# Performance work log

Hardware: AMD Instinct MI355X
Metric: run time of the kernel (lower is better)

## Reference

```python
import jax, jax.numpy as jnp
import numpy as np
import math

T_MIN = 0.1
T_MAX = 1.0


def setup_inputs() -> dict:
    key = jax.random.key(0)
    k1, k2, k3, k4, k5, k6 = jax.random.split(key, 6)
    B, H, SQ, SK, DK = 1, 16, 4096, 4096, 64
    query = jax.random.normal(k1, (B, H, SQ, DK), dtype=jnp.float32)
    key_t = jax.random.normal(k2, (B, H, SK, DK), dtype=jnp.float32)
    # MLP params (3 -> 16 -> 1). Original zero-inits the last layer; we use
    # small random values so gradients flow to query/key in the bwd test.
    W1 = jax.random.normal(k3, (16, 3), dtype=jnp.float32) * 0.5
    b1 = jax.random.normal(k4, (16,), dtype=jnp.float32) * 0.1
    W2 = jax.random.normal(k5, (1, 16), dtype=jnp.float32) * 0.5
    b2 = jax.random.normal(k6, (1,), dtype=jnp.float32) * 0.1
    return {"query": query, "key": key_t, "W1": W1, "b1": b1, "W2": W2, "b2": b2}


def reference(query, key, W1, b1, W2, b2):
    d_k = query.shape[-1]
    sk = key.shape[-2]
    q = query.astype(jnp.float32)
    k = key.astype(jnp.float32)
    # [B,H,Sq,Sk] score matrix
    scores = jnp.einsum('bhqd,bhkd->bhqk', q, k) / math.sqrt(d_k)
    scores = jnp.clip(scores, -50.0, 50.0)
    mean_sim = scores.mean(axis=(-2, -1))                 # [B,H]
    max_sim = scores.max(axis=-1).mean(axis=-1)           # [B,H]
    probs = jax.nn.softmax(scores / 2.0, axis=-1)         # [B,H,Sq,Sk]
    # torch .var(dim=-1) is unbiased (divisor Sk-1)
    pm = probs.mean(axis=-1, keepdims=True)
    var = ((probs - pm) ** 2).sum(axis=-1) / (sk - 1)     # [B,H,Sq]
    entropy_proxy = var.mean(axis=-1)                     # [B,H]
    mean_sim = jnp.clip(mean_sim, -10.0, 10.0)
    max_sim = jnp.clip(max_sim, -10.0, 10.0)
    entropy_proxy = jnp.clip(entropy_proxy, 0.0, 1.0)
    features = jnp.stack([mean_sim, max_sim, entropy_proxy], axis=-1)  # [B,H,3]
    h = jnp.tanh(features @ W1.T + b1)
    raw_t = h @ W2.T + b2                                 # [B,H,1]
    t = T_MIN + jax.nn.sigmoid(raw_t) * (T_MAX - T_MIN)
    t = jnp.clip(t, T_MIN, T_MAX)
    return t[..., None].astype(query.dtype)               # [B,H,1,1]
```

## Files before the change

### kernel.cpp

```cpp
#include <hip/hip_runtime.h>
#include <math.h>

#define NH   16
#define SQL  4096
#define SKL  4096
#define DK   64
#define QB   128
#define KB   64
#define KSPLIT 2
#define KHALF (SKL / KSPLIT)
#define NKT   (KHALF / KB)

#define QSCALE  0.090168440f
#define UNSCALE 1.3862943611f

#define NB2      (NH * 32 * KSPLIT)
#define ROWFLOAT (NB2 * QB)

typedef __bf16 bf16x8 __attribute__((ext_vector_type(8)));
typedef __bf16 bf16x4 __attribute__((ext_vector_type(4)));
typedef float  f32x4  __attribute__((ext_vector_type(4)));
typedef float  f32x2  __attribute__((ext_vector_type(2)));

#if __has_builtin(__builtin_amdgcn_exp2f)
#define EXP2(x) __builtin_amdgcn_exp2f(x)
#else
#define EXP2(x) exp2f(x)
#endif

static __device__ __forceinline__ f32x2 pk_fma(f32x2 a, f32x2 b, f32x2 c) {
#if __has_builtin(__builtin_elementwise_fma)
    return __builtin_elementwise_fma(a, b, c);
#else
    f32x2 r; r[0] = fmaf(a[0], b[0], c[0]); r[1] = fmaf(a[1], b[1], c[1]); return r;
#endif
}
static __device__ __forceinline__ f32x2 pk_max(f32x2 a, f32x2 b) {
#if __has_builtin(__builtin_elementwise_max)
    return __builtin_elementwise_max(a, b);
#else
    f32x2 r; r[0] = fmaxf(a[0], b[0]); r[1] = fmaxf(a[1], b[1]); return r;
#endif
}

__device__ __forceinline__ int swz(int row, int col_bytes) {
    return ((row << 7) + col_bytes) ^ ((row & 7) << 4);
}

__global__ __launch_bounds__(512, 8) void dtp_stats_mfma(const float* __restrict__ Q,
                                                         const float* __restrict__ K,
                                                         float* __restrict__ RSUM,
                                                         float* __restrict__ RMX,
                                                         float* __restrict__ RS1,
                                                         float* __restrict__ RS2) {
    __shared__ __align__(16) unsigned char Qs[QB * DK * 2];
    __shared__ __align__(16) unsigned char Ks[2][KB * DK * 2];
    __shared__ float red[32];

    const int qb   = blockIdx.x;
    const int h    = blockIdx.y;
    const int half = blockIdx.z;
    const int tid  = threadIdx.x;
    const int lane = tid & 63;
    const int w    = tid >> 6;
    const int l15  = lane & 15;
    const int lg   = lane >> 4;

    const float* Qh = Q + ((size_t)h * SQL + (size_t)qb * QB) * DK;
    const float* Kh = K + ((size_t)h * SKL + (size_t)half * KHALF) * DK;

    const int sc4 = tid & 15;
    const int sr0 = tid >> 4;

    #pragma unroll
    for (int j = 0; j < 4; ++j) {
        int r = sr0 + 32 * j;
        const float4 v = *reinterpret_cast<const float4*>(Qh + r * DK + sc4 * 4);
        bf16x4 hv;
        hv[0] = (__bf16)(v.x * QSCALE); hv[1] = (__bf16)(v.y * QSCALE);
        hv[2] = (__bf16)(v.z * QSCALE); hv[3] = (__bf16)(v.w * QSCALE);
        *reinterpret_cast<bf16x4*>(&Qs[swz(r, sc4 * 8)]) = hv;
    }

    float4 kreg[2];
    #pragma unroll
    for (int j = 0; j < 2; ++j)
        kreg[j] = *reinterpret_cast<const float4*>(Kh + (size_t)(sr0 + 32 * j) * DK + sc4 * 4);
    #pragma unroll
    for (int j = 0; j < 2; ++j) {
        int r = sr0 + 32 * j;
        bf16x4 hv;
        hv[0] = (__bf16)kreg[j].x; hv[1] = (__bf16)kreg[j].y;
        hv[2] = (__bf16)kreg[j].z; hv[3] = (__bf16)kreg[j].w;
        *reinterpret_cast<bf16x4*>(&Ks[0][swz(r, sc4 * 8)]) = hv;
    }
    #pragma unroll
    for (int j = 0; j < 2; ++j)
        kreg[j] = *reinterpret_cast<const float4*>(Kh + (size_t)(KB + sr0 + 32 * j) * DK + sc4 * 4);

    __syncthreads();

    bf16x8 aF[2];
    {
        int r = w * 16 + l15;
        aF[0] = *reinterpret_cast<const bf16x8*>(&Qs[swz(r, 0 * 64 + lg * 16)]);
        aF[1] = *reinterpret_cast<const bf16x8*>(&Qs[swz(r, 1 * 64 + lg * 16)]);
    }

    f32x2 rsum01 = {0.f, 0.f}, rsum23 = {0.f, 0.f};
    f32x2 rmx01  = {-3.0e38f, -3.0e38f}, rmx23 = {-3.0e38f, -3.0e38f};
    f32x2 rs1_01 = {0.f, 0.f}, rs1_23 = {0.f, 0.f};
    f32x2 rs2_01 = {0.f, 0.f}, rs2_23 = {0.f, 0.f};

    for (int kt = 0; kt < NKT; ++kt) {
        const int cur = kt & 1;

        if (kt + 1 < NKT) {
            #pragma unroll
            for (int j = 0; j < 2; ++j) {
                int r = sr0 + 32 * j;
                bf16x4 hv;
                hv[0] = (__bf16)kreg[j].x; hv[1] = (__bf16)kreg[j].y;
                hv[2] = (__bf16)kreg[j].z; hv[3] = (__bf16)kreg[j].w;
                *reinterpret_cast<bf16x4*>(&Ks[cur ^ 1][swz(r, sc4 * 8)]) = hv;
            }
            if (kt + 2 < NKT) {
                const float* Kt = Kh + (size_t)(kt + 2) * KB * DK;
                #pragma unroll
                for (int j = 0; j < 2; ++j)
                    kreg[j] = *reinterpret_cast<const float4*>(Kt + (size_t)(sr0 + 32 * j) * DK + sc4 * 4);
            }
        }

        f32x4 acc[4];
        #pragma unroll
        for (int ct = 0; ct < 4; ++ct) {
            int rr = ct * 16 + l15;
            bf16x8 b0 = *reinterpret_cast<const bf16x8*>(&Ks[cur][swz(rr, 0 * 64 + lg * 16)]);
            bf16x8 b1 = *reinterpret_cast<const bf16x8*>(&Ks[cur][swz(rr, 1 * 64 + lg * 16)]);
            f32x4 a = {0.f, 0.f, 0.f, 0.f};
            a = __builtin_amdgcn_mfma_f32_16x16x32_bf16(aF[0], b0, a, 0, 0, 0);
            a = __builtin_amdgcn_mfma_f32_16x16x32_bf16(aF[1], b1, a, 0, 0, 0);
            acc[ct] = a;
        }

        #pragma unroll
        for (int ct = 0; ct < 4; ++ct) {
            f32x2 v01 = __builtin_shufflevector(acc[ct], acc[ct], 0, 1);
            f32x2 v23 = __builtin_shufflevector(acc[ct], acc[ct], 2, 3);
            rsum01 += v01; rsum23 += v23;
            rmx01 = pk_max(rmx01, v01);
            rmx23 = pk_max(rmx23, v23);
            f32x2 e01, e23;
            e01[0] = EXP2(v01[0]); e01[1] = EXP2(v01[1]);
            e23[0] = EXP2(v23[0]); e23[1] = EXP2(v23[1]);
            rs1_01 += e01; rs1_23 += e23;
            rs2_01 = pk_fma(e01, e01, rs2_01);
            rs2_23 = pk_fma(e23, e23, rs2_23);
        }

        __syncthreads();
    }

    #pragma unroll
    for (int m = 1; m < 16; m <<= 1) {
        #pragma unroll
        for (int c = 0; c < 2; ++c) {
            rsum01[c] += __shfl_xor(rsum01[c], m, 64);
            rsum23[c] += __shfl_xor(rsum23[c], m, 64);
            rmx01[c]   = fmaxf(rmx01[c], __shfl_xor(rmx01[c], m, 64));
            rmx23[c]   = fmaxf(rmx23[c], __shfl_xor(rmx23[c], m, 64));
            rs1_01[c] += __shfl_xor(rs1_01[c], m, 64);
            rs1_23[c] += __shfl_xor(rs1_23[c], m, 64);
            rs2_01[c] += __shfl_xor(rs2_01[c], m, 64);
            rs2_23[c] += __shfl_xor(rs2_23[c], m, 64);
        }
    }

    const int base = (h * 32 + qb) * KSPLIT + half;
    if (l15 == 0) {
        const size_t rb = (size_t)base * QB + (w * 16 + lg * 4);
        float4 mx = {rmx01[0] * UNSCALE, rmx01[1] * UNSCALE,
                     rmx23[0] * UNSCALE, rmx23[1] * UNSCALE};
        float4 s1 = {rs1_01[0], rs1_01[1], rs1_23[0], rs1_23[1]};
        float4 s2 = {rs2_01[0], rs2_01[1], rs2_23[0], rs2_23[1]};
        *reinterpret_cast<float4*>(&RMX[rb]) = mx;
        *reinterpret_cast<float4*>(&RS1[rb]) = s1;
        *reinterpret_cast<float4*>(&RS2[rb]) = s2;
        red[w * 4 + lg] = (rsum01[0] + rsum01[1]) + (rsum23[0] + rsum23[1]);
    }
    __syncthreads();
    if (tid == 0) {
        float bs = 0.f;
        #pragma unroll
        for (int i = 0; i < 32; ++i) bs += red[i];
        RSUM[base] = bs * UNSCALE;
    }
}

__global__ __launch_bounds__(256) void dtp_finalize(const float* __restrict__ RSUM,
                                                    const float* __restrict__ RMX,
                                                    const float* __restrict__ RS1,
                                                    const float* __restrict__ RS2,
                                                    const float* __restrict__ W1,
                                                    const float* __restrict__ b1,
                                                    const float* __restrict__ W2,
                                                    const float* __restrict__ b2,
                                                    float* __restrict__ out) {
    const int h   = blockIdx.x;
    const int tid = threadIdx.x;
    const float invSK  = 1.0f / (float)SKL;
    const float invSK1 = 1.0f / (float)(SKL - 1);

    float sm = 0.f, sv = 0.f;
    #pragma unroll
    for (int j = 0; j < 16; ++j) {
        int r  = tid + 256 * j;
        int qb = r >> 7;
        int rr = r & 127;
        size_t b0 = ((size_t)(h * 32 + qb) * KSPLIT) * QB + rr;
        size_t b1i = b0 + QB;
        float mx = fmaxf(RMX[b0], RMX[b1i]);
        float s1 = RS1[b0] + RS1[b1i];
        float s2 = RS2[b0] + RS2[b1i];
        sm += mx;
        sv += (s2 / (s1 * s1) - invSK) * invSK1;
    }

    float ss = (tid < NH * 0 + 64) ? RSUM[h * 64 + (tid & 63)] : 0.f;
    if (tid >= 64) ss = 0.f;

    #pragma unroll
    for (int m = 1; m < 64; m <<= 1) {
        sm += __shfl_xor(sm, m, 64);
        sv += __shfl_xor(sv, m, 64);
        ss += __shfl_xor(ss, m, 64);
    }
    __shared__ float redm[4], redv[4], reds[4];
    const int wv = tid >> 6;
    if ((tid & 63) == 0) { redm[wv] = sm; redv[wv] = sv; reds[wv] = ss; }
    __syncthreads();

    if (tid == 0) {
        float tsm = redm[0] + redm[1] + redm[2] + redm[3];
        float tsv = redv[0] + redv[1] + redv[2] + redv[3];
        float tss = reds[0];
        float mean_sim = tss / ((float)SQL * (float)SKL);
        float max_sim  = tsm / (float)SQL;
        float entropy  = tsv / (float)SQL;
        mean_sim = fminf(fmaxf(mean_sim, -10.f), 10.f);
        max_sim  = fminf(fmaxf(max_sim,  -10.f), 10.f);
        entropy  = fminf(fmaxf(entropy,    0.f), 1.f);
        float raw = b2[0];
        #pragma unroll
        for (int i = 0; i < 16; ++i) {
            float a = b1[i] + W1[i*3+0] * mean_sim + W1[i*3+1] * max_sim + W1[i*3+2] * entropy;
            raw += W2[i] * tanhf(a);
        }
        float t = 0.1f + 0.9f / (1.0f + __expf(-raw));
        t = fminf(fmaxf(t, 0.1f), 1.0f);
        out[h] = t;
    }
}

extern "C" void kernel_launch(void* const* d_in, const int* in_sizes, int n_in,
                              void* d_out, int out_size, void* d_ws, size_t ws_size,
                              hipStream_t stream) {
    const float* Q  = (const float*)d_in[0];
    const float* K  = (const float*)d_in[1];
    const float* W1 = (const float*)d_in[2];
    const float* b1 = (const float*)d_in[3];
    const float* W2 = (const float*)d_in[4];
    const float* b2 = (const float*)d_in[5];
    float* out      = (float*)d_out;

    float* RSUM = (float*)d_ws;
    float* RMX  = RSUM + NB2;
    float* RS1  = RMX + ROWFLOAT;
    float* RS2  = RS1 + ROWFLOAT;

    dim3 grid(SQL / QB, NH, KSPLIT);
    dtp_stats_mfma<<<grid, 512, 0, stream>>>(Q, K, RSUM, RMX, RS1, RS2);
    dtp_finalize<<<NH, 256, 0, stream>>>(RSUM, RMX, RS1, RS2, W1, b1, W2, b2, out);
}
```

Before: 77.72 us.

## Prepack Q/K to swizzled bf16 and stream tiles with global_load_lds

Adds a prepack kernel that converts Q and K to bf16 once, already in the swizzled LDS tile layout, and writes them to workspace. The stats kernel then copies tiles straight from global memory into LDS with global_load_lds, so it no longer converts through registers. It also runs 256 threads per block with each wave covering two 16-row Q tiles, which reuses each K fragment twice. This costs an extra kernel launch and a round trip through workspace for the packed data. It falls back to the old register path when the workspace is too small.

```diff
diff --git a/kernel.cpp b/kernel.cpp
--- a/kernel.cpp
+++ b/kernel.cpp
@@ -16,6 +16,12 @@
 
 #define NB2      (NH * 32 * KSPLIT)
 #define ROWFLOAT (NB2 * QB)
+#define STATS_BYTES ((size_t)(NB2 + 3 * ROWFLOAT) * 4)
+
+#define KIMG 8192
+#define QIMG 16384
+#define KPRE_BYTES ((size_t)NH * 64 * KIMG)
+#define QPRE_BYTES ((size_t)NH * 32 * QIMG)
 
 typedef __bf16 bf16x8 __attribute__((ext_vector_type(8)));
 typedef __bf16 bf16x4 __attribute__((ext_vector_type(4)));
@@ -47,14 +53,56 @@
     return ((row << 7) + col_bytes) ^ ((row & 7) << 4);
 }
 
-__global__ __launch_bounds__(512, 8) void dtp_stats_mfma(const float* __restrict__ Q,
-                                                         const float* __restrict__ K,
+static __device__ __forceinline__ void gld16(void* l, const void* g) {
+#if __has_builtin(__builtin_amdgcn_global_load_lds)
+    __builtin_amdgcn_global_load_lds(
+        (const __attribute__((address_space(1))) unsigned int*)g,
+        (__attribute__((address_space(3))) unsigned int*)l,
+        16, 0, 0);
+#else
+    *reinterpret_cast<float4*>(l) = *reinterpret_cast<const float4*>(g);
+#endif
+}
+
+__global__ __launch_bounds__(512) void dtp_prepack(const float* __restrict__ Q,
+                                                   const float* __restrict__ K,
+                                                   unsigned char* __restrict__ Qpre,
+                                                   unsigned char* __restrict__ Kpre) {
+    const int i   = blockIdx.x * 512 + threadIdx.x;
+    const int c16 = i & 7;
+    const int rg  = i >> 3;
+    const int h   = rg >> 12;
+    const int row = rg & 4095;
+
+    const float* ks = K + (size_t)rg * DK + c16 * 8;
+    float4 a = *reinterpret_cast<const float4*>(ks);
+    float4 b = *reinterpret_cast<const float4*>(ks + 4);
+    bf16x8 kv;
+    kv[0]=(__bf16)a.x; kv[1]=(__bf16)a.y; kv[2]=(__bf16)a.z; kv[3]=(__bf16)a.w;
+    kv[4]=(__bf16)b.x; kv[5]=(__bf16)b.y; kv[6]=(__bf16)b.z; kv[7]=(__bf16)b.w;
+    *reinterpret_cast<bf16x8*>(
+        &Kpre[(size_t)h * 64 * KIMG + (size_t)(row >> 6) * KIMG + swz(row & 63, c16 * 16)]) = kv;
+
+    const float* qs = Q + (size_t)rg * DK + c16 * 8;
+    float4 c = *reinterpret_cast<const float4*>(qs);
+    float4 d = *reinterpret_cast<const float4*>(qs + 4);
+    bf16x8 qv;
+    qv[0]=(__bf16)(c.x*QSCALE); qv[1]=(__bf16)(c.y*QSCALE);
+    qv[2]=(__bf16)(c.z*QSCALE); qv[3]=(__bf16)(c.w*QSCALE);
+    qv[4]=(__bf16)(d.x*QSCALE); qv[5]=(__bf16)(d.y*QSCALE);
+    qv[6]=(__bf16)(d.z*QSCALE); qv[7]=(__bf16)(d.w*QSCALE);
+    *reinterpret_cast<bf16x8*>(
+        &Qpre[(size_t)h * 32 * QIMG + (size_t)(row >> 7) * QIMG + swz(row & 127, c16 * 16)]) = qv;
+}
+
+__global__ __launch_bounds__(256, 4) void dtp_stats_glds(const unsigned char* __restrict__ Qpre,
+                                                         const unsigned char* __restrict__ Kpre,
                                                          float* __restrict__ RSUM,
                                                          float* __restrict__ RMX,
                                                          float* __restrict__ RS1,
                                                          float* __restrict__ RS2) {
-    __shared__ __align__(16) unsigned char Qs[QB * DK * 2];
-    __shared__ __align__(16) unsigned char Ks[2][KB * DK * 2];
+    __shared__ __align__(16) unsigned char Qs[QIMG];
+    __shared__ __align__(16) unsigned char Ks[2][KIMG];
     __shared__ float red[32];
 
     const int qb   = blockIdx.x;
@@ -66,29 +114,153 @@
     const int l15  = lane & 15;
     const int lg   = lane >> 4;
 
+    const unsigned char* Qg = Qpre + (size_t)(h * 32 + qb) * QIMG;
+    const unsigned char* Kg = Kpre + (size_t)h * 64 * KIMG + (size_t)half * NKT * KIMG;
+
+    {
+        const int off = tid * 16;
+        #pragma unroll
+        for (int r2 = 0; r2 < 4; ++r2)
+            gld16(&Qs[off + r2 * 4096], Qg + off + r2 * 4096);
+        gld16(&Ks[0][off],        Kg + off);
+        gld16(&Ks[0][off + 4096], Kg + off + 4096);
+    }
+    __syncthreads();
+
+    bf16x8 aF[2][2];
+    #pragma unroll
+    for (int rt = 0; rt < 2; ++rt) {
+        int r = w * 32 + rt * 16 + l15;
+        aF[rt][0] = *reinterpret_cast<const bf16x8*>(&Qs[swz(r, 0 * 64 + lg * 16)]);
+        aF[rt][1] = *reinterpret_cast<const bf16x8*>(&Qs[swz(r, 1 * 64 + lg * 16)]);
+    }
+
+    f32x2 rsum[2][2], rmx[2][2], rs1[2][2], rs2[2][2];
+    #pragma unroll
+    for (int rt = 0; rt < 2; ++rt)
+        #pragma unroll
+        for (int p = 0; p < 2; ++p) {
+            rsum[rt][p] = (f32x2){0.f, 0.f};
+            rmx[rt][p]  = (f32x2){-3.0e38f, -3.0e38f};
+            rs1[rt][p]  = (f32x2){0.f, 0.f};
+            rs2[rt][p]  = (f32x2){0.f, 0.f};
+        }
+
+    for (int t = 0; t < NKT; ++t) {
+        const int b = t & 1;
+
+        if (t + 1 < NKT) {
+            const unsigned char* Kt = Kg + (size_t)(t + 1) * KIMG;
+            const int off = tid * 16;
+            gld16(&Ks[b ^ 1][off],        Kt + off);
+            gld16(&Ks[b ^ 1][off + 4096], Kt + off + 4096);
+        }
+
+        #pragma unroll
+        for (int ct = 0; ct < 4; ++ct) {
+            int rr = ct * 16 + l15;
+            bf16x8 b0 = *reinterpret_cast<const bf16x8*>(&Ks[b][swz(rr, 0 * 64 + lg * 16)]);
+            bf16x8 b1 = *reinterpret_cast<const bf16x8*>(&Ks[b][swz(rr, 1 * 64 + lg * 16)]);
+            #pragma unroll
+            for (int rt = 0; rt < 2; ++rt) {
+                f32x4 a = {0.f, 0.f, 0.f, 0.f};
+                a = __builtin_amdgcn_mfma_f32_16x16x32_bf16(aF[rt][0], b0, a, 0, 0, 0);
+                a = __builtin_amdgcn_mfma_f32_16x16x32_bf16(aF[rt][1], b1, a, 0, 0, 0);
+                f32x2 v01 = __builtin_shufflevector(a, a, 0, 1);
+                f32x2 v23 = __builtin_shufflevector(a, a, 2, 3);
+                rsum[rt][0] += v01; rsum[rt][1] += v23;
+                rmx[rt][0] = pk_max(rmx[rt][0], v01);
+                rmx[rt][1] = pk_max(rmx[rt][1], v23);
+                f32x2 e01, e23;
+                e01[0] = EXP2(v01[0]); e01[1] = EXP2(v01[1]);
+                e23[0] = EXP2(v23[0]); e23[1] = EXP2(v23[1]);
+                rs1[rt][0] += e01; rs1[rt][1] += e23;
+                rs2[rt][0] = pk_fma(e01, e01, rs2[rt][0]);
+                rs2[rt][1] = pk_fma(e23, e23, rs2[rt][1]);
+            }
+        }
+
+        __syncthreads();
+    }
+
+    #pragma unroll
+    for (int m = 1; m < 16; m <<= 1) {
+        #pragma unroll
+        for (int rt = 0; rt < 2; ++rt)
+            #pragma unroll
+            for (int c = 0; c < 2; ++c) {
+                rsum[rt][c][0] += __shfl_xor(rsum[rt][c][0], m, 64);
+                rsum[rt][c][1] += __shfl_xor(rsum[rt][c][1], m, 64);
+                rmx[rt][c][0]   = fmaxf(rmx[rt][c][0], __shfl_xor(rmx[rt][c][0], m, 64));
+                rmx[rt][c][1]   = fmaxf(rmx[rt][c][1], __shfl_xor(rmx[rt][c][1], m, 64));
+                rs1[rt][c][0]  += __shfl_xor(rs1[rt][c][0], m, 64);
+                rs1[rt][c][1]  += __shfl_xor(rs1[rt][c][1], m, 64);
+                rs2[rt][c][0]  += __shfl_xor(rs2[rt][c][0], m, 64);
+                rs2[rt][c][1]  += __shfl_xor(rs2[rt][c][1], m, 64);
+            }
+    }
+
+    const int base = (h * 32 + qb) * KSPLIT + half;
+    if (l15 == 0) {
+        float bs = 0.f;
+        #pragma unroll
+        for (int rt = 0; rt < 2; ++rt) {
+            const size_t rb = (size_t)base * QB + (w * 32 + rt * 16 + lg * 4);
+            float4 mx = {rmx[rt][0][0] * UNSCALE, rmx[rt][0][1] * UNSCALE,
+                         rmx[rt][1][0] * UNSCALE, rmx[rt][1][1] * UNSCALE};
+            float4 s1 = {rs1[rt][0][0], rs1[rt][0][1], rs1[rt][1][0], rs1[rt][1][1]};
+            float4 s2 = {rs2[rt][0][0], rs2[rt][0][1], rs2[rt][1][0], rs2[rt][1][1]};
+            *reinterpret_cast<float4*>(&RMX[rb]) = mx;
+            *reinterpret_cast<float4*>(&RS1[rb]) = s1;
+            *reinterpret_cast<float4*>(&RS2[rb]) = s2;
+            bs += (rsum[rt][0][0] + rsum[rt][0][1]) + (rsum[rt][1][0] + rsum[rt][1][1]);
+        }
+        red[w * 8 + lg * 2 + 0] = bs;
+        red[w * 8 + lg * 2 + 1] = 0.f;
+    }
+    __syncthreads();
+    if (tid == 0) {
+        float bs = 0.f;
+        #pragma unroll
+        for (int i = 0; i < 32; ++i) bs += red[i];
+        RSUM[base] = bs * UNSCALE;
+    }
+}
+
+__global__ __launch_bounds__(512, 8) void dtp_stats_reg(const float* __restrict__ Q,
+                                                        const float* __restrict__ K,
+                                                        float* __restrict__ RSUM,
+                                                        float* __restrict__ RMX,
+                                                        float* __restrict__ RS1,
+                                                        float* __restrict__ RS2) {
+    __shared__ __align__(16) unsigned char Qs[QB * DK * 2];
+    __shared__ __align__(16) unsigned char Ks[2][KB * DK * 2];
+    __shared__ float red[32];
+
+    const int qb = blockIdx.x, h = blockIdx.y, half = blockIdx.z;
+    const int tid = threadIdx.x, lane = tid & 63, w = tid >> 6;
+    const int l15 = lane & 15, lg = lane >> 4;
+
     const float* Qh = Q + ((size_t)h * SQL + (size_t)qb * QB) * DK;
     const float* Kh = K + ((size_t)h * SKL + (size_t)half * KHALF) * DK;
-
-    const int sc4 = tid & 15;
-    const int sr0 = tid >> 4;
+    const int sc4 = tid & 15, sr = tid >> 4;
 
     #pragma unroll
     for (int j = 0; j < 4; ++j) {
-        int r = sr0 + 32 * j;
+        int r = sr + 32 * j;
         const float4 v = *reinterpret_cast<const float4*>(Qh + r * DK + sc4 * 4);
         bf16x4 hv;
         hv[0] = (__bf16)(v.x * QSCALE); hv[1] = (__bf16)(v.y * QSCALE);
         hv[2] = (__bf16)(v.z * QSCALE); hv[3] = (__bf16)(v.w * QSCALE);
         *reinterpret_cast<bf16x4*>(&Qs[swz(r, sc4 * 8)]) = hv;
     }
-
     float4 kreg[2];
     #pragma unroll
     for (int j = 0; j < 2; ++j)
-        kreg[j] = *reinterpret_cast<const float4*>(Kh + (size_t)(sr0 + 32 * j) * DK + sc4 * 4);
+        kreg[j] = *reinterpret_cast<const float4*>(Kh + (size_t)(sr + 32 * j) * DK + sc4 * 4);
     #pragma unroll
     for (int j = 0; j < 2; ++j) {
-        int r = sr0 + 32 * j;
+        int r = sr + 32 * j;
         bf16x4 hv;
         hv[0] = (__bf16)kreg[j].x; hv[1] = (__bf16)kreg[j].y;
         hv[2] = (__bf16)kreg[j].z; hv[3] = (__bf16)kreg[j].w;
@@ -96,8 +268,7 @@
     }
     #pragma unroll
     for (int j = 0; j < 2; ++j)
-        kreg[j] = *reinterpret_cast<const float4*>(Kh + (size_t)(KB + sr0 + 32 * j) * DK + sc4 * 4);
-
+        kreg[j] = *reinterpret_cast<const float4*>(Kh + (size_t)(KB + sr + 32 * j) * DK + sc4 * 4);
     __syncthreads();
 
     bf16x8 aF[2];
@@ -106,19 +277,17 @@
         aF[0] = *reinterpret_cast<const bf16x8*>(&Qs[swz(r, 0 * 64 + lg * 16)]);
         aF[1] = *reinterpret_cast<const bf16x8*>(&Qs[swz(r, 1 * 64 + lg * 16)]);
     }
-
-    f32x2 rsum01 = {0.f, 0.f}, rsum23 = {0.f, 0.f};
-    f32x2 rmx01  = {-3.0e38f, -3.0e38f}, rmx23 = {-3.0e38f, -3.0e38f};
-    f32x2 rs1_01 = {0.f, 0.f}, rs1_23 = {0.f, 0.f};
-    f32x2 rs2_01 = {0.f, 0.f}, rs2_23 = {0.f, 0.f};
+    f32x2 rsum01 = {0.f,0.f}, rsum23 = {0.f,0.f};
+    f32x2 rmx01 = {-3.0e38f,-3.0e38f}, rmx23 = {-3.0e38f,-3.0e38f};
+    f32x2 rs1_01 = {0.f,0.f}, rs1_23 = {0.f,0.f};
+    f32x2 rs2_01 = {0.f,0.f}, rs2_23 = {0.f,0.f};
 
     for (int kt = 0; kt < NKT; ++kt) {
         const int cur = kt & 1;
-
         if (kt + 1 < NKT) {
             #pragma unroll
             for (int j = 0; j < 2; ++j) {
-                int r = sr0 + 32 * j;
+                int r = sr + 32 * j;
                 bf16x4 hv;
                 hv[0] = (__bf16)kreg[j].x; hv[1] = (__bf16)kreg[j].y;
                 hv[2] = (__bf16)kreg[j].z; hv[3] = (__bf16)kreg[j].w;
@@ -128,11 +297,9 @@
                 const float* Kt = Kh + (size_t)(kt + 2) * KB * DK;
                 #pragma unroll
                 for (int j = 0; j < 2; ++j)
-                    kreg[j] = *reinterpret_cast<const float4*>(Kt + (size_t)(sr0 + 32 * j) * DK + sc4 * 4);
+                    kreg[j] = *reinterpret_cast<const float4*>(Kt + (size_t)(sr + 32 * j) * DK + sc4 * 4);
             }
         }
-
-        f32x4 acc[4];
         #pragma unroll
         for (int ct = 0; ct < 4; ++ct) {
             int rr = ct * 16 + l15;
@@ -141,16 +308,10 @@
             f32x4 a = {0.f, 0.f, 0.f, 0.f};
             a = __builtin_amdgcn_mfma_f32_16x16x32_bf16(aF[0], b0, a, 0, 0, 0);
             a = __builtin_amdgcn_mfma_f32_16x16x32_bf16(aF[1], b1, a, 0, 0, 0);
-            acc[ct] = a;
-        }
-
-        #pragma unroll
-        for (int ct = 0; ct < 4; ++ct) {
-            f32x2 v01 = __builtin_shufflevector(acc[ct], acc[ct], 0, 1);
-            f32x2 v23 = __builtin_shufflevector(acc[ct], acc[ct], 2, 3);
+            f32x2 v01 = __builtin_shufflevector(a, a, 0, 1);
+            f32x2 v23 = __builtin_shufflevector(a, a, 2, 3);
             rsum01 += v01; rsum23 += v23;
-            rmx01 = pk_max(rmx01, v01);
-            rmx23 = pk_max(rmx23, v23);
+            rmx01 = pk_max(rmx01, v01); rmx23 = pk_max(rmx23, v23);
             f32x2 e01, e23;
             e01[0] = EXP2(v01[0]); e01[1] = EXP2(v01[1]);
             e23[0] = EXP2(v23[0]); e23[1] = EXP2(v23[1]);
@@ -158,30 +319,26 @@
             rs2_01 = pk_fma(e01, e01, rs2_01);
             rs2_23 = pk_fma(e23, e23, rs2_23);
         }
-
         __syncthreads();
     }
-
     #pragma unroll
     for (int m = 1; m < 16; m <<= 1) {
         #pragma unroll
         for (int c = 0; c < 2; ++c) {
             rsum01[c] += __shfl_xor(rsum01[c], m, 64);
             rsum23[c] += __shfl_xor(rsum23[c], m, 64);
-            rmx01[c]   = fmaxf(rmx01[c], __shfl_xor(rmx01[c], m, 64));
-            rmx23[c]   = fmaxf(rmx23[c], __shfl_xor(rmx23[c], m, 64));
+            rmx01[c] = fmaxf(rmx01[c], __shfl_xor(rmx01[c], m, 64));
+            rmx23[c] = fmaxf(rmx23[c], __shfl_xor(rmx23[c], m, 64));
             rs1_01[c] += __shfl_xor(rs1_01[c], m, 64);
             rs1_23[c] += __shfl_xor(rs1_23[c], m, 64);
             rs2_01[c] += __shfl_xor(rs2_01[c], m, 64);
             rs2_23[c] += __shfl_xor(rs2_23[c], m, 64);
         }
     }
-
     const int base = (h * 32 + qb) * KSPLIT + half;
     if (l15 == 0) {
         const size_t rb = (size_t)base * QB + (w * 16 + lg * 4);
-        float4 mx = {rmx01[0] * UNSCALE, rmx01[1] * UNSCALE,
-                     rmx23[0] * UNSCALE, rmx23[1] * UNSCALE};
+        float4 mx = {rmx01[0]*UNSCALE, rmx01[1]*UNSCALE, rmx23[0]*UNSCALE, rmx23[1]*UNSCALE};
         float4 s1 = {rs1_01[0], rs1_01[1], rs1_23[0], rs1_23[1]};
         float4 s2 = {rs2_01[0], rs2_01[1], rs2_23[0], rs2_23[1]};
         *reinterpret_cast<float4*>(&RMX[rb]) = mx;
@@ -218,7 +375,7 @@
         int r  = tid + 256 * j;
         int qb = r >> 7;
         int rr = r & 127;
-        size_t b0 = ((size_t)(h * 32 + qb) * KSPLIT) * QB + rr;
+        size_t b0  = ((size_t)(h * 32 + qb) * KSPLIT) * QB + rr;
         size_t b1i = b0 + QB;
         float mx = fmaxf(RMX[b0], RMX[b1i]);
         float s1 = RS1[b0] + RS1[b1i];
@@ -226,10 +383,7 @@
         sm += mx;
         sv += (s2 / (s1 * s1) - invSK) * invSK1;
     }
-
-    float ss = (tid < NH * 0 + 64) ? RSUM[h * 64 + (tid & 63)] : 0.f;
-    if (tid >= 64) ss = 0.f;
-
+    float ss = (tid < 64) ? RSUM[h * 64 + (tid & 63)] : 0.f;
     #pragma unroll
     for (int m = 1; m < 64; m <<= 1) {
         sm += __shfl_xor(sm, m, 64);
@@ -240,7 +394,6 @@
     const int wv = tid >> 6;
     if ((tid & 63) == 0) { redm[wv] = sm; redv[wv] = sv; reds[wv] = ss; }
     __syncthreads();
-
     if (tid == 0) {
         float tsm = redm[0] + redm[1] + redm[2] + redm[3];
         float tsv = redv[0] + redv[1] + redv[2] + redv[3];
@@ -279,7 +432,16 @@
     float* RS1  = RMX + ROWFLOAT;
     float* RS2  = RS1 + ROWFLOAT;
 
+    const size_t need = STATS_BYTES + QPRE_BYTES + KPRE_BYTES;
     dim3 grid(SQL / QB, NH, KSPLIT);
-    dtp_stats_mfma<<<grid, 512, 0, stream>>>(Q, K, RSUM, RMX, RS1, RS2);
+
+    if (ws_size >= need) {
+        unsigned char* Qpre = (unsigned char*)d_ws + STATS_BYTES;
+        unsigned char* Kpre = Qpre + QPRE_BYTES;
+        dtp_prepack<<<1024, 512, 0, stream>>>(Q, K, Qpre, Kpre);
+        dtp_stats_glds<<<grid, 256, 0, stream>>>(Qpre, Kpre, RSUM, RMX, RS1, RS2);
+    } else {
+        dtp_stats_reg<<<grid, 512, 0, stream>>>(Q, K, RSUM, RMX, RS1, RS2);
+    }
     dtp_finalize<<<NH, 256, 0, stream>>>(RSUM, RMX, RS1, RS2, W1, b1, W2, b2, out);
 }
```

After: 76.93 us. Within noise of the previous version (-1.0%).
